# Kernel optimization log

Measured on AMD Instinct MI355X. Metric: run time of the kernel, lower is better.

Reference implementation:

```python
import jax, jax.numpy as jnp
import numpy as np

N_NODES = 50000
HEADS1 = 4
NEG_SLOPE = 0.2
EPS = 1e-16


def gat_conv(x, edge_index, W, att_src, att_dst, bias, heads, out_ch, concat):
    # edge_index: [2, E] with self-loops already appended by caller
    src, dst = edge_index[0], edge_index[1]
    N = x.shape[0]
    h = (x @ W).reshape(N, heads, out_ch)                      # [N, H, C]
    a_src = jnp.sum(h * att_src, axis=-1)                      # [N, H]
    a_dst = jnp.sum(h * att_dst, axis=-1)                      # [N, H]
    e = a_src[src] + a_dst[dst]                                # [E, H]
    e = jnp.where(e > 0, e, NEG_SLOPE * e)                     # leaky_relu
    m = jax.ops.segment_max(e, dst, num_segments=N)            # [N, H]
    alpha = jnp.exp(e - m[dst])                                # [E, H]
    denom = jax.ops.segment_sum(alpha, dst, num_segments=N)    # [N, H]
    alpha = alpha / (denom[dst] + EPS)                         # [E, H]
    msg = alpha[:, :, None] * h[src]                           # [E, H, C]
    out = jax.ops.segment_sum(msg, dst, num_segments=N)        # [N, H, C]
    if concat:
        out = out.reshape(N, heads * out_ch)
    else:
        out = out.mean(axis=1)
    return out + bias, alpha


def setup_inputs() -> dict:
    key = jax.random.key(0)
    ks = jax.random.split(key, 12)
    N, F, H, heads, C, E = N_NODES, 256, 64, HEADS1, 40, 800000
    g = 0.1
    return {
        "x": jax.random.normal(ks[0], (N, F), dtype=jnp.float32),
        "edge_index": jax.random.randint(ks[1], (2, E), 0, N, dtype=jnp.int32),
        "W1": jax.random.normal(ks[2], (F, heads * H), dtype=jnp.float32) * g,
        "att_src1": jax.random.normal(ks[3], (heads, H), dtype=jnp.float32) * g,
        "att_dst1": jax.random.normal(ks[4], (heads, H), dtype=jnp.float32) * g,
        "b1": jnp.zeros((heads * H,), dtype=jnp.float32),
        "W2": jax.random.normal(ks[5], (heads * H, C), dtype=jnp.float32) * g,
        "att_src2": jax.random.normal(ks[6], (1, C), dtype=jnp.float32) * g,
        "att_dst2": jax.random.normal(ks[7], (1, C), dtype=jnp.float32) * g,
        "b2": jnp.zeros((C,), dtype=jnp.float32),
    }


def reference(x, edge_index, W1, att_src1, att_dst1, b1, W2, att_src2, att_dst2, b2):
    N = x.shape[0]
    # add self-loops (PyG GATConv default)
    loops = jnp.arange(N, dtype=edge_index.dtype)
    ei = jnp.concatenate([edge_index, jnp.stack([loops, loops])], axis=1)
    # dropout is identity in eval mode
    h1, alpha = gat_conv(x, ei, W1, att_src1, att_dst1, b1,
                         HEADS1, W1.shape[1] // HEADS1, concat=True)
    h1 = jax.nn.elu(h1)
    h2, _ = gat_conv(h1, ei, W2, att_src2, att_dst2, b2,
                     1, W2.shape[1], concat=False)
    return jax.nn.log_softmax(h2, axis=1), alpha
```

## Files before the change

### kernel.cpp

```cpp
#include <hip/hip_runtime.h>
#include <math.h>

#define N_NODES 50000
#define HC1 256
#define H1 4
#define C2 40
#define C2P 64
#define E0 800000
#define ET 850000
#define NEG_SLOPE 0.2f
#define EPS_A 1e-16f

typedef __bf16 bf16x8 __attribute__((ext_vector_type(8)));
typedef float f32x4 __attribute__((ext_vector_type(4)));
typedef unsigned short u16x8 __attribute__((ext_vector_type(8)));


__device__ inline unsigned short f2bf(float f) {
    unsigned u = __float_as_uint(f);
    return (unsigned short)((u + 0x7FFFu + ((u >> 16) & 1u)) >> 16);
}
__device__ inline float bf2f(unsigned short h) { return __uint_as_float(((unsigned)h) << 16); }
__device__ inline float bf_lo(unsigned q) { return __uint_as_float(q << 16); }
__device__ inline float bf_hi(unsigned q) { return __uint_as_float(q & 0xFFFF0000u); }


__global__ void fill_int_kernel(int* __restrict__ p, int n, int v) {
    int i = blockIdx.x * blockDim.x + threadIdx.x;
    if (i < n) p[i] = v;
}

__device__ inline int edge_src(const int* __restrict__ ei, int e) {
    return (e < E0) ? ei[e] : (e - E0);
}
__device__ inline int edge_dst(const int* __restrict__ ei, int e) {
    return (e < E0) ? ei[E0 + e] : (e - E0);
}


__global__ void f32_to_bf16_kernel(const float* __restrict__ src,
                                   unsigned short* __restrict__ dst, int n4) {
    int i = blockIdx.x * blockDim.x + threadIdx.x;
    if (i >= n4) return;
    float4 v = ((const float4*)src)[i];
    ushort4 w;
    w.x = f2bf(v.x); w.y = f2bf(v.y); w.z = f2bf(v.z); w.w = f2bf(v.w);
    ((ushort4*)dst)[i] = w;
}

__global__ void w1_transpose_kernel(const float* __restrict__ W1,
                                    unsigned short* __restrict__ Wt) {
    int tid = blockIdx.x * blockDim.x + threadIdx.x;
    if (tid >= 256 * 256) return;
    int n = tid >> 8, k = tid & 255;
    Wt[tid] = f2bf(W1[k * 256 + n]);
}

__global__ void w2_transpose_pad_kernel(const float* __restrict__ W2,
                                        unsigned short* __restrict__ Wt) {
    int tid = blockIdx.x * blockDim.x + threadIdx.x;
    if (tid >= 64 * 256) return;
    int n = tid >> 8, k = tid & 255;
    Wt[tid] = (n < C2) ? f2bf(W2[k * C2 + n]) : (unsigned short)0;
}


__global__ void hist_kernel(const int* __restrict__ ei, int* __restrict__ deg) {
    int e = blockIdx.x * blockDim.x + threadIdx.x;
    if (e >= ET) return;
    atomicAdd(&deg[edge_dst(ei, e)], 1);
}

__global__ __launch_bounds__(256) void scan_block_kernel(const int* __restrict__ deg,
                                                         int* __restrict__ excl,
                                                         int* __restrict__ bsum) {
    __shared__ int tmp[256];
    int t = threadIdx.x;
    int i = blockIdx.x * 256 + t;
    int v = (i < N_NODES) ? deg[i] : 0;
    tmp[t] = v;
    __syncthreads();
#pragma unroll
    for (int o = 1; o < 256; o <<= 1) {
        int x = (t >= o) ? tmp[t - o] : 0;
        __syncthreads();
        tmp[t] += x;
        __syncthreads();
    }
    if (i < N_NODES) excl[i] = tmp[t] - v;
    if (t == 255) bsum[blockIdx.x] = tmp[255];
}

#define NSCAN_B 196

__global__ __launch_bounds__(256) void scan_top_kernel(int* __restrict__ bsum) {
    __shared__ int tmp[256];
    int t = threadIdx.x;
    int v = (t < NSCAN_B) ? bsum[t] : 0;
    tmp[t] = v;
    __syncthreads();
#pragma unroll
    for (int o = 1; o < 256; o <<= 1) {
        int x = (t >= o) ? tmp[t - o] : 0;
        __syncthreads();
        tmp[t] += x;
        __syncthreads();
    }
    if (t < NSCAN_B) bsum[t] = tmp[t] - v;
}

__global__ __launch_bounds__(256) void scan_add_kernel(int* __restrict__ offsets,
                                                       int* __restrict__ cursor,
                                                       const int* __restrict__ bsum) {
    int i = blockIdx.x * 256 + threadIdx.x;
    if (i < N_NODES) {
        int v = offsets[i] + bsum[blockIdx.x];
        offsets[i] = v;
        cursor[i] = v;
    }
    if (i == 0) offsets[N_NODES] = ET;
}

__global__ void scatter_kernel(const int* __restrict__ ei, int* __restrict__ cursor,
                               int2* __restrict__ csr_es) {
    int e = blockIdx.x * blockDim.x + threadIdx.x;
    if (e >= ET) return;
    int d = edge_dst(ei, e);
    int pos = atomicAdd(&cursor[d], 1);
    csr_es[pos] = make_int2(e, edge_src(ei, e));
}


template <int TBM, int TBN, int WROWS, int WCOLS>
__global__ __launch_bounds__(256) void gemm_mfma_kernel(const unsigned short* __restrict__ Abf,
                                                        const unsigned short* __restrict__ Bt,
                                                        unsigned short* __restrict__ Cbf,
                                                        const float* __restrict__ att_s,
                                                        const float* __restrict__ att_d,
                                                        float* __restrict__ a_src_o,
                                                        float* __restrict__ a_dst_o,
                                                        int M, int Nc, int attN, int hstride) {
    static_assert(TBM == WROWS * 64 && TBN == WCOLS * 64, "tile");
    constexpr int LDK = 40;
    __shared__ alignas(16) unsigned short As[TBM * LDK];
    __shared__ alignas(16) unsigned short Bs[TBN * LDK];
    const int t = threadIdx.x;
    const int lane = t & 63;
    const int w = t >> 6;
    const int quad = lane >> 4;
    const int l16 = lane & 15;
    const int wm = (w / WCOLS) * 64;
    const int wn = (w % WCOLS) * 64;
    const int bm = blockIdx.x * TBM;
    const int bn = blockIdx.y * TBN;

    f32x4 acc[4][4] = {};

    for (int k0 = 0; k0 < 256; k0 += 32) {
        __syncthreads();
#pragma unroll
        for (int i = 0; i < TBM / 64; ++i) {
            int idx = t + i * 256;
            int row = idx >> 2, seg = idx & 3;
            u16x8 v = {};
            if (bm + row < M)
                v = *(const u16x8*)(Abf + (size_t)(bm + row) * 256 + k0 + seg * 8);
            *(u16x8*)&As[row * LDK + seg * 8] = v;
        }
#pragma unroll
        for (int i = 0; i < TBN / 64; ++i) {
            int idx = t + i * 256;
            int row = idx >> 2, seg = idx & 3;
            u16x8 v = *(const u16x8*)(Bt + (size_t)(bn + row) * 256 + k0 + seg * 8);
            *(u16x8*)&Bs[row * LDK + seg * 8] = v;
        }
        __syncthreads();

        bf16x8 af[4], bfr[4];
#pragma unroll
        for (int mi = 0; mi < 4; ++mi)
            af[mi] = *(const bf16x8*)&As[(wm + mi * 16 + l16) * LDK + quad * 8];
#pragma unroll
        for (int ni = 0; ni < 4; ++ni)
            bfr[ni] = *(const bf16x8*)&Bs[(wn + ni * 16 + l16) * LDK + quad * 8];
#pragma unroll
        for (int mi = 0; mi < 4; ++mi)
#pragma unroll
            for (int ni = 0; ni < 4; ++ni)
                acc[mi][ni] = __builtin_amdgcn_mfma_f32_16x16x32_bf16(
                    af[mi], bfr[ni], acc[mi][ni], 0, 0, 0);
    }

#pragma unroll
    for (int mi = 0; mi < 4; ++mi)
#pragma unroll
        for (int ni = 0; ni < 4; ++ni)
#pragma unroll
            for (int r = 0; r < 4; ++r) {
                int row = bm + wm + mi * 16 + quad * 4 + r;
                int col = bn + wn + ni * 16 + l16;
                if (row < M)
                    Cbf[(size_t)row * Nc + col] = f2bf(acc[mi][ni][r]);
            }

    float asc[4], adc[4];
#pragma unroll
    for (int ni = 0; ni < 4; ++ni) {
        int col = bn + wn + ni * 16 + l16;
        bool valid = col < attN;
        asc[ni] = valid ? att_s[col] : 0.f;
        adc[ni] = valid ? att_d[col] : 0.f;
    }
    float vs[16], vd[16];
#pragma unroll
    for (int mi = 0; mi < 4; ++mi)
#pragma unroll
        for (int r = 0; r < 4; ++r) {
            float s = 0.f, dd = 0.f;
#pragma unroll
            for (int ni = 0; ni < 4; ++ni) {
                s += acc[mi][ni][r] * asc[ni];
                dd += acc[mi][ni][r] * adc[ni];
            }
            vs[mi * 4 + r] = s;
            vd[mi * 4 + r] = dd;
        }
#pragma unroll
    for (int k = 0; k < 4; ++k) {
        const int o = 1 << k;
        const int b = (l16 >> k) & 1;
#pragma unroll
        for (int j = 0; j < (8 >> k); ++j) {
            float lo = vs[2 * j], hi = vs[2 * j + 1];
            float keep = b ? hi : lo, send = b ? lo : hi;
            vs[j] = keep + __shfl_xor(send, o);
            lo = vd[2 * j]; hi = vd[2 * j + 1];
            keep = b ? hi : lo; send = b ? lo : hi;
            vd[j] = keep + __shfl_xor(send, o);
        }
    }
    {
        int mi = l16 >> 2, r = l16 & 3;
        int row = bm + wm + mi * 16 + quad * 4 + r;
        int head = (bn + wn) >> 6;
        if (row < M) {
            a_src_o[(size_t)row * hstride + head] = vs[0];
            a_dst_o[(size_t)row * hstride + head] = vd[0];
        }
    }
}


#define DCAP 512
__global__ __launch_bounds__(256) void l1_fused_kernel(const int* __restrict__ off,
                                                       const int2* __restrict__ csr_es,
                                                       const float* __restrict__ a_src,
                                                       const float* __restrict__ a_dst,
                                                       const unsigned* __restrict__ h1bf,
                                                       const float* __restrict__ b1,
                                                       float* __restrict__ alpha_out,
                                                       unsigned* __restrict__ out1bf) {
    __shared__ int   s_src[DCAP];
    __shared__ float s_al[DCAP][5];
    __shared__ float s_stat[4][2];
    __shared__ float s_comb[2][128][2];
    int d = blockIdx.x;
    int t = threadIdx.x;
    int hd = t >> 6, lane = t & 63;
    int beg = off[d], end = off[d + 1];
    int deg = end - beg;
    float ad = a_dst[d * H1 + hd];

    float elc[8];
    float mx = -INFINITY;
    int c = 0;
    for (int idx = beg + lane; idx < end; idx += 64, ++c) {
        int2 es = csr_es[idx];
        int j = idx - beg;
        if (hd == 0 && j < DCAP) s_src[j] = es.y;
        float el = a_src[es.y * H1 + hd] + ad;
        el = el > 0.f ? el : NEG_SLOPE * el;
        if (c < 8) elc[c] = el;
        mx = fmaxf(mx, el);
    }
#pragma unroll
    for (int o = 32; o; o >>= 1) mx = fmaxf(mx, __shfl_xor(mx, o));

    float sum = 0.f;
    c = 0;
    for (int idx = beg + lane; idx < end; idx += 64, ++c) {
        float el;
        if (c < 8) el = elc[c];
        else {
            int2 es = csr_es[idx];
            el = a_src[es.y * H1 + hd] + ad;
            el = el > 0.f ? el : NEG_SLOPE * el;
        }
        sum += expf(el - mx);
    }
#pragma unroll
    for (int o = 32; o; o >>= 1) sum += __shfl_xor(sum, o);
    float inv = 1.f / (sum + EPS_A);
    if (lane == 0) { s_stat[hd][0] = mx; s_stat[hd][1] = inv; }

    c = 0;
    for (int idx = beg + lane; idx < end; idx += 64, ++c) {
        int2 es = csr_es[idx];
        float el;
        if (c < 8) el = elc[c];
        else {
            el = a_src[es.y * H1 + hd] + ad;
            el = el > 0.f ? el : NEG_SLOPE * el;
        }
        float a = expf(el - mx) * inv;
        alpha_out[(size_t)es.x * H1 + hd] = a;
        int j = idx - beg;
        if (j < DCAP) s_al[j][hd] = a;
    }
    __syncthreads();

    int tt = t & 127, eo = t >> 7, head = tt >> 5;
    float acc0 = 0.f, acc1 = 0.f;
    int n = min(deg, DCAP);
    int j = eo;
    for (; j + 6 < n; j += 8) {
        int s0 = s_src[j], s1 = s_src[j + 2], s2 = s_src[j + 4], s3 = s_src[j + 6];
        float a0 = s_al[j][head], a1 = s_al[j + 2][head];
        float a2 = s_al[j + 4][head], a3 = s_al[j + 6][head];
        unsigned q0 = h1bf[(size_t)s0 * 128 + tt];
        unsigned q1 = h1bf[(size_t)s1 * 128 + tt];
        unsigned q2 = h1bf[(size_t)s2 * 128 + tt];
        unsigned q3 = h1bf[(size_t)s3 * 128 + tt];
        acc0 += a0 * bf_lo(q0) + a1 * bf_lo(q1) + a2 * bf_lo(q2) + a3 * bf_lo(q3);
        acc1 += a0 * bf_hi(q0) + a1 * bf_hi(q1) + a2 * bf_hi(q2) + a3 * bf_hi(q3);
    }
    for (; j < n; j += 2) {
        unsigned q = h1bf[(size_t)s_src[j] * 128 + tt];
        float a = s_al[j][head];
        acc0 += a * bf_lo(q);
        acc1 += a * bf_hi(q);
    }
    for (int jj = DCAP + eo; jj < deg; jj += 2) {
        int2 es = csr_es[beg + jj];
        float el = a_src[es.y * H1 + head] + a_dst[d * H1 + head];
        el = el > 0.f ? el : NEG_SLOPE * el;
        float a = expf(el - s_stat[head][0]) * s_stat[head][1];
        unsigned q = h1bf[(size_t)es.y * 128 + tt];
        acc0 += a * bf_lo(q);
        acc1 += a * bf_hi(q);
    }
    s_comb[eo][tt][0] = acc0;
    s_comb[eo][tt][1] = acc1;
    __syncthreads();
    if (t < 128) {
        float2 bb = *(const float2*)&b1[2 * t];
        float v0 = s_comb[0][t][0] + s_comb[1][t][0] + bb.x;
        float v1 = s_comb[0][t][1] + s_comb[1][t][1] + bb.y;
        v0 = v0 > 0.f ? v0 : expm1f(v0);
        v1 = v1 > 0.f ? v1 : expm1f(v1);
        out1bf[(size_t)d * 128 + t] = ((unsigned)f2bf(v1) << 16) | (unsigned)f2bf(v0);
    }
}


__global__ __launch_bounds__(256) void l2_fused_kernel(const int* __restrict__ off,
                                                       const int2* __restrict__ csr_es,
                                                       const float* __restrict__ a_src,
                                                       const float* __restrict__ a_dst,
                                                       const unsigned* __restrict__ h2bf,
                                                       const float* __restrict__ b2,
                                                       float* __restrict__ out) {
    int t = threadIdx.x;
    int lane = t & 63;
    int d = blockIdx.x * 4 + (t >> 6);
    if (d >= N_NODES) return;
    int beg = off[d], end = off[d + 1];
    int deg = end - beg;
    float ad = a_dst[d];
    int nch = (deg + 63) >> 6;

    float elc[4]; int sc[4];
    float mx = -INFINITY;
    for (int cc = 0; cc < nch; ++cc) {
        int idx = beg + cc * 64 + lane;
        float el = -INFINITY; int s = 0;
        if (idx < end) {
            int2 es = csr_es[idx];
            s = es.y;
            el = a_src[s] + ad;
            el = el > 0.f ? el : NEG_SLOPE * el;
        }
        if (cc < 4) { elc[cc] = el; sc[cc] = s; }
        mx = fmaxf(mx, el);
    }
#pragma unroll
    for (int o = 32; o; o >>= 1) mx = fmaxf(mx, __shfl_xor(mx, o));

    float sum = 0.f;
    for (int cc = 0; cc < nch; ++cc) {
        float el;
        if (cc < 4) el = elc[cc];
        else {
            int idx = beg + cc * 64 + lane;
            el = -INFINITY;
            if (idx < end) {
                int2 es = csr_es[idx];
                el = a_src[es.y] + ad;
                el = el > 0.f ? el : NEG_SLOPE * el;
            }
        }
        sum += expf(el - mx);
    }
#pragma unroll
    for (int o = 32; o; o >>= 1) sum += __shfl_xor(sum, o);
    float inv = 1.f / (sum + EPS_A);

    int half = lane >> 5, li = lane & 31;
    float acc0 = 0.f, acc1 = 0.f;
    for (int cc = 0; cc < nch; ++cc) {
        int cnt = min(64, deg - cc * 64);
        int my_s; float my_a;
        if (cc < 4) {
            my_s = sc[cc];
            my_a = expf(elc[cc] - mx) * inv;
        } else {
            int idx = beg + cc * 64 + lane;
            my_s = 0; my_a = 0.f;
            if (idx < end) {
                int2 es = csr_es[idx];
                my_s = es.y;
                float el = a_src[es.y] + ad;
                el = el > 0.f ? el : NEG_SLOPE * el;
                my_a = expf(el - mx) * inv;
            }
        }
        for (int j = 0; j < cnt; j += 2) {
            int jj = j + half;
            int s = __shfl(my_s, jj);
            float a = __shfl(my_a, jj);
            if (jj < cnt) {
                unsigned q = h2bf[(size_t)s * 32 + li];
                acc0 += a * bf_lo(q);
                acc1 += a * bf_hi(q);
            }
        }
    }
    acc0 += __shfl_xor(acc0, 32);
    acc1 += __shfl_xor(acc1, 32);
    bool act = li < 20;
    float v0 = act ? acc0 + b2[2 * li]     : -INFINITY;
    float v1 = act ? acc1 + b2[2 * li + 1] : -INFINITY;
    float mmx = fmaxf(v0, v1);
#pragma unroll
    for (int o = 16; o; o >>= 1) mmx = fmaxf(mmx, __shfl_xor(mmx, o));
    float ex = act ? expf(v0 - mmx) + expf(v1 - mmx) : 0.f;
#pragma unroll
    for (int o = 16; o; o >>= 1) ex += __shfl_xor(ex, o);
    float ls = logf(ex);
    if (act && half == 0)
        *(float2*)&out[(size_t)d * C2 + 2 * li] = make_float2(v0 - mmx - ls, v1 - mmx - ls);
}


extern "C" void kernel_launch(void* const* d_in, const int* in_sizes, int n_in,
                              void* d_out, int out_size, void* d_ws, size_t ws_size,
                              hipStream_t stream) {
    const float* x   = (const float*)d_in[0];
    const int*   ei  = (const int*)d_in[1];
    const float* W1  = (const float*)d_in[2];
    const float* as1 = (const float*)d_in[3];
    const float* ad1 = (const float*)d_in[4];
    const float* b1  = (const float*)d_in[5];
    const float* W2  = (const float*)d_in[6];
    const float* as2 = (const float*)d_in[7];
    const float* ad2 = (const float*)d_in[8];
    const float* b2  = (const float*)d_in[9];

    float* out   = (float*)d_out;
    float* alpha = out + (size_t)N_NODES * C2;

    unsigned* u32    = (unsigned*)d_ws;
    unsigned* h1bf   = u32;
    unsigned* xbf    = h1bf + 6400000;
    unsigned* h2bf   = xbf + 6400000;
    unsigned* w1t    = h2bf + 1600000;
    unsigned* w2t    = w1t + 32768;
    float* a_src1    = (float*)(w2t + 8192);
    float* a_dst1    = a_src1 + 200000;
    float* a_src2    = a_dst1 + 200000;
    float* a_dst2    = a_src2 + 50000;
    int*   deg       = (int*)(a_dst2 + 50000);
    int*   offs      = deg + 50000;
    int*   cursor    = offs + 50001;
    int*   bsum      = cursor + 50000;
    int2*  csr_es    = (int2*)(bsum + 257);
    unsigned* out1bf = xbf;

    const int TB = 256;
    const int EB = (ET + TB - 1) / TB;

    fill_int_kernel<<<(N_NODES + TB - 1) / TB, TB, 0, stream>>>(deg, N_NODES, 0);
    hist_kernel<<<EB, TB, 0, stream>>>(ei, deg);
    scan_block_kernel<<<NSCAN_B, TB, 0, stream>>>(deg, offs, bsum);
    scan_top_kernel<<<1, TB, 0, stream>>>(bsum);
    scan_add_kernel<<<NSCAN_B, TB, 0, stream>>>(offs, cursor, bsum);
    scatter_kernel<<<EB, TB, 0, stream>>>(ei, cursor, csr_es);

    f32_to_bf16_kernel<<<(3200000 + TB - 1) / TB, TB, 0, stream>>>(
        x, (unsigned short*)xbf, 3200000);
    w1_transpose_kernel<<<(65536 + TB - 1) / TB, TB, 0, stream>>>(W1, (unsigned short*)w1t);
    w2_transpose_pad_kernel<<<(16384 + TB - 1) / TB, TB, 0, stream>>>(W2, (unsigned short*)w2t);

    gemm_mfma_kernel<128, 128, 2, 2><<<dim3((N_NODES + 127) / 128, 2), TB, 0, stream>>>(
        (const unsigned short*)xbf, (const unsigned short*)w1t, (unsigned short*)h1bf,
        as1, ad1, a_src1, a_dst1, N_NODES, HC1, 256, H1);
    l1_fused_kernel<<<N_NODES, TB, 0, stream>>>(offs, csr_es, a_src1, a_dst1,
                                                h1bf, b1, alpha, out1bf);

    gemm_mfma_kernel<256, 64, 4, 1><<<dim3((N_NODES + 255) / 256, 1), TB, 0, stream>>>(
        (const unsigned short*)out1bf, (const unsigned short*)w2t, (unsigned short*)h2bf,
        as2, ad2, a_src2, a_dst2, N_NODES, C2P, C2, 1);
    l2_fused_kernel<<<(N_NODES + 3) / 4, TB, 0, stream>>>(offs, csr_es, a_src2, a_dst2,
                                                          h2bf, b2, out);
}
```

Measured before the change: 423.5 us.

## Cache softmax numerators in LDS, defer normalization, vectorize alpha stores, use fast exp

In the layer-1 fused kernel, unnormalized exp values are stored in shared memory during the sum pass. The separate third pass that recomputed exp is removed, and alpha is written as one float4 per edge (all four heads) using stored edge ids. Normalization by 1/sum is moved to after aggregation in both layers. expf, expm1f and logf are replaced with the fast intrinsics. This removes redundant exp work and scattered scalar alpha writes, at the cost of an extra block barrier, more LDS, and slightly lower accuracy in exp and ELU near zero.

Measured after the change: 414.2 us. 2.2% less time.

```diff
diff --git a/kernel.cpp b/kernel.cpp
--- a/kernel.cpp
+++ b/kernel.cpp
@@ -261,8 +261,9 @@
                                                        float* __restrict__ alpha_out,
                                                        unsigned* __restrict__ out1bf) {
     __shared__ int   s_src[DCAP];
-    __shared__ float s_al[DCAP][5];
-    __shared__ float s_stat[4][2];
+    __shared__ int   s_eid[DCAP];
+    __shared__ float s_al[H1][DCAP];
+    __shared__ float s_stat[H1][2];
     __shared__ float s_comb[2][128][2];
     int d = blockIdx.x;
     int t = threadIdx.x;
@@ -277,7 +278,7 @@
     for (int idx = beg + lane; idx < end; idx += 64, ++c) {
         int2 es = csr_es[idx];
         int j = idx - beg;
-        if (hd == 0 && j < DCAP) s_src[j] = es.y;
+        if (hd == 0 && j < DCAP) { s_src[j] = es.y; s_eid[j] = es.x; }
         float el = a_src[es.y * H1 + hd] + ad;
         el = el > 0.f ? el : NEG_SLOPE * el;
         if (c < 8) elc[c] = el;
@@ -296,37 +297,40 @@
             el = a_src[es.y * H1 + hd] + ad;
             el = el > 0.f ? el : NEG_SLOPE * el;
         }
-        sum += expf(el - mx);
+        float p = __expf(el - mx);
+        int j = idx - beg;
+        if (j < DCAP) s_al[hd][j] = p;
+        sum += p;
     }
 #pragma unroll
     for (int o = 32; o; o >>= 1) sum += __shfl_xor(sum, o);
     float inv = 1.f / (sum + EPS_A);
     if (lane == 0) { s_stat[hd][0] = mx; s_stat[hd][1] = inv; }
-
-    c = 0;
-    for (int idx = beg + lane; idx < end; idx += 64, ++c) {
+    __syncthreads();
+
+    int n = min(deg, DCAP);
+    {
+        float i0 = s_stat[0][1], i1 = s_stat[1][1], i2 = s_stat[2][1], i3 = s_stat[3][1];
+        for (int j = t; j < n; j += 256) {
+            float4 a4 = make_float4(s_al[0][j] * i0, s_al[1][j] * i1,
+                                    s_al[2][j] * i2, s_al[3][j] * i3);
+            *(float4*)&alpha_out[(size_t)s_eid[j] * H1] = a4;
+        }
+    }
+    for (int idx = beg + DCAP + lane; idx < end; idx += 64) {
         int2 es = csr_es[idx];
-        float el;
-        if (c < 8) el = elc[c];
-        else {
-            el = a_src[es.y * H1 + hd] + ad;
-            el = el > 0.f ? el : NEG_SLOPE * el;
-        }
-        float a = expf(el - mx) * inv;
-        alpha_out[(size_t)es.x * H1 + hd] = a;
-        int j = idx - beg;
-        if (j < DCAP) s_al[j][hd] = a;
-    }
-    __syncthreads();
+        float el = a_src[es.y * H1 + hd] + ad;
+        el = el > 0.f ? el : NEG_SLOPE * el;
+        alpha_out[(size_t)es.x * H1 + hd] = __expf(el - mx) * inv;
+    }
 
     int tt = t & 127, eo = t >> 7, head = tt >> 5;
     float acc0 = 0.f, acc1 = 0.f;
-    int n = min(deg, DCAP);
     int j = eo;
     for (; j + 6 < n; j += 8) {
         int s0 = s_src[j], s1 = s_src[j + 2], s2 = s_src[j + 4], s3 = s_src[j + 6];
-        float a0 = s_al[j][head], a1 = s_al[j + 2][head];
-        float a2 = s_al[j + 4][head], a3 = s_al[j + 6][head];
+        float a0 = s_al[head][j], a1 = s_al[head][j + 2];
+        float a2 = s_al[head][j + 4], a3 = s_al[head][j + 6];
         unsigned q0 = h1bf[(size_t)s0 * 128 + tt];
         unsigned q1 = h1bf[(size_t)s1 * 128 + tt];
         unsigned q2 = h1bf[(size_t)s2 * 128 + tt];
@@ -336,7 +340,7 @@
     }
     for (; j < n; j += 2) {
         unsigned q = h1bf[(size_t)s_src[j] * 128 + tt];
-        float a = s_al[j][head];
+        float a = s_al[head][j];
         acc0 += a * bf_lo(q);
         acc1 += a * bf_hi(q);
     }
@@ -344,20 +348,21 @@
         int2 es = csr_es[beg + jj];
         float el = a_src[es.y * H1 + head] + a_dst[d * H1 + head];
         el = el > 0.f ? el : NEG_SLOPE * el;
-        float a = expf(el - s_stat[head][0]) * s_stat[head][1];
+        float p = __expf(el - s_stat[head][0]);
         unsigned q = h1bf[(size_t)es.y * 128 + tt];
-        acc0 += a * bf_lo(q);
-        acc1 += a * bf_hi(q);
+        acc0 += p * bf_lo(q);
+        acc1 += p * bf_hi(q);
     }
     s_comb[eo][tt][0] = acc0;
     s_comb[eo][tt][1] = acc1;
     __syncthreads();
     if (t < 128) {
+        float invh = s_stat[t >> 5][1];
         float2 bb = *(const float2*)&b1[2 * t];
-        float v0 = s_comb[0][t][0] + s_comb[1][t][0] + bb.x;
-        float v1 = s_comb[0][t][1] + s_comb[1][t][1] + bb.y;
-        v0 = v0 > 0.f ? v0 : expm1f(v0);
-        v1 = v1 > 0.f ? v1 : expm1f(v1);
+        float v0 = (s_comb[0][t][0] + s_comb[1][t][0]) * invh + bb.x;
+        float v1 = (s_comb[0][t][1] + s_comb[1][t][1]) * invh + bb.y;
+        v0 = v0 > 0.f ? v0 : __expf(v0) - 1.f;
+        v1 = v1 > 0.f ? v1 : __expf(v1) - 1.f;
         out1bf[(size_t)d * 128 + t] = ((unsigned)f2bf(v1) << 16) | (unsigned)f2bf(v0);
     }
 }
@@ -398,18 +403,21 @@
 
     float sum = 0.f;
     for (int cc = 0; cc < nch; ++cc) {
-        float el;
-        if (cc < 4) el = elc[cc];
-        else {
+        float p;
+        if (cc < 4) {
+            p = __expf(elc[cc] - mx);
+            elc[cc] = p;
+        } else {
             int idx = beg + cc * 64 + lane;
-            el = -INFINITY;
+            float el = -INFINITY;
             if (idx < end) {
                 int2 es = csr_es[idx];
                 el = a_src[es.y] + ad;
                 el = el > 0.f ? el : NEG_SLOPE * el;
             }
-        }
-        sum += expf(el - mx);
+            p = __expf(el - mx);
+        }
+        sum += p;
     }
 #pragma unroll
     for (int o = 32; o; o >>= 1) sum += __shfl_xor(sum, o);
@@ -422,7 +430,7 @@
         int my_s; float my_a;
         if (cc < 4) {
             my_s = sc[cc];
-            my_a = expf(elc[cc] - mx) * inv;
+            my_a = elc[cc];
         } else {
             int idx = beg + cc * 64 + lane;
             my_s = 0; my_a = 0.f;
@@ -431,7 +439,7 @@
                 my_s = es.y;
                 float el = a_src[es.y] + ad;
                 el = el > 0.f ? el : NEG_SLOPE * el;
-                my_a = expf(el - mx) * inv;
+                my_a = __expf(el - mx);
             }
         }
         for (int j = 0; j < cnt; j += 2) {
@@ -447,16 +455,18 @@
     }
     acc0 += __shfl_xor(acc0, 32);
     acc1 += __shfl_xor(acc1, 32);
+    acc0 *= inv;
+    acc1 *= inv;
     bool act = li < 20;
     float v0 = act ? acc0 + b2[2 * li]     : -INFINITY;
     float v1 = act ? acc1 + b2[2 * li + 1] : -INFINITY;
     float mmx = fmaxf(v0, v1);
 #pragma unroll
     for (int o = 16; o; o >>= 1) mmx = fmaxf(mmx, __shfl_xor(mmx, o));
-    float ex = act ? expf(v0 - mmx) + expf(v1 - mmx) : 0.f;
+    float ex = act ? __expf(v0 - mmx) + __expf(v1 - mmx) : 0.f;
 #pragma unroll
     for (int o = 16; o; o >>= 1) ex += __shfl_xor(ex, o);
-    float ls = logf(ex);
+    float ls = __logf(ex);
     if (act && half == 0)
         *(float2*)&out[(size_t)d * C2 + 2 * li] = make_float2(v0 - mmx - ls, v1 - mmx - ls);
 }
```
